# Kernel tuning notes

Hardware: AMD Instinct MI355X
Metric: run time of the kernel (lower is better)

The kernel has to match this reference:

```python
import jax, jax.numpy as jnp
import numpy as np

K_CONST = 0.005
D_U = 0.001
D_V = 0.005
LAYERS = [3, 256, 256, 256, 256, 2]
N_PTS = 131072


def setup_inputs() -> dict:
    key = jax.random.key(0)
    ks = jax.random.split(key, 3 + 2 * (len(LAYERS) - 1))
    inp = {
        "t": jax.random.uniform(ks[0], (N_PTS, 1), dtype=jnp.float32),
        "x": jax.random.uniform(ks[1], (N_PTS, 1), dtype=jnp.float32),
        "y": jax.random.uniform(ks[2], (N_PTS, 1), dtype=jnp.float32),
    }
    # PyTorch nn.Linear default init: U(-1/sqrt(fan_in), 1/sqrt(fan_in))
    for i in range(len(LAYERS) - 1):
        fan_in = LAYERS[i]
        s = 1.0 / np.sqrt(fan_in)
        inp[f"W{i}"] = jax.random.uniform(ks[3 + 2 * i], (LAYERS[i], LAYERS[i + 1]),
                                          minval=-s, maxval=s, dtype=jnp.float32)
        inp[f"b{i}"] = jax.random.uniform(ks[4 + 2 * i], (LAYERS[i + 1],),
                                          minval=-s, maxval=s, dtype=jnp.float32)
    return inp


def _mlp(params, inp):
    # inp: (3,) -> (2,) tanh MLP (tanh on all but last layer)
    h = inp
    for W, b in params[:-1]:
        h = jnp.tanh(h @ W + b)
    W, b = params[-1]
    return h @ W + b


def reference(t, x, y, W0, b0, W1, b1, W2, b2, W3, b3, W4, b4):
    params = [(W0, b0), (W1, b1), (W2, b2), (W3, b3), (W4, b4)]
    net = lambda p: _mlp(params, p)  # (3,) -> (2,)

    pts = jnp.concatenate([t, x, y], axis=1)            # (N, 3)
    uv = jax.vmap(net)(pts)                              # (N, 2)
    jac = jax.vmap(jax.jacrev(net))(pts)                 # (N, 2, 3)
    hess = jax.vmap(jax.jacfwd(jax.jacrev(net)))(pts)    # (N, 2, 3, 3)

    u = uv[:, 0:1]
    v = uv[:, 1:2]
    u_t = jac[:, 0, 0:1]
    v_t = jac[:, 1, 0:1]
    u_xx = hess[:, 0, 1, 1][:, None]
    u_yy = hess[:, 0, 2, 2][:, None]
    v_xx = hess[:, 1, 1, 1][:, None]
    v_yy = hess[:, 1, 2, 2][:, None]

    f = u - u ** 3 - K_CONST - v + D_U * (u_xx + u_yy) - u_t
    g = u - v + D_V * (v_xx + v_yy) - v_t
    return (u, v, f, g)
```

## Files before the change

kernel.cpp:

```cpp
#include <hip/hip_runtime.h>
#include <math.h>

#define N_PTS   131072
#define K_CONST 0.005f
#define D_U     0.001f
#define D_V     0.005f

typedef unsigned short u16;
typedef __attribute__((ext_vector_type(8))) _Float16 f16x8;
typedef __attribute__((ext_vector_type(4))) float    f32x4;
typedef __attribute__((ext_vector_type(4))) u16      u16x4;
typedef __attribute__((ext_vector_type(8))) u16      u16x8;

__device__ __forceinline__ u16 f2h(float x){
    _Float16 h = (_Float16)x;
    return __builtin_bit_cast(u16, h);
}
__device__ __forceinline__ float h2f(u16 h){
    return (float)__builtin_bit_cast(_Float16, h);
}

__device__ __forceinline__ float tanh_fast(float z){
    float e = __expf(2.f * z);
    return 1.f - 2.f * __builtin_amdgcn_rcpf(e + 1.f);
}

__global__ void prep_weights(const float* __restrict__ W1, const float* __restrict__ W2,
                             const float* __restrict__ W3, u16* __restrict__ ws)
{
    int gid  = blockIdx.x * 256 + threadIdx.x;
    int lane = gid & 63;
    int nt   = (gid >> 6) & 15;
    int ks   = (gid >> 10) & 7;
    int L    = gid >> 13;
    if (L >= 3) return;
    const float* W = (L == 0) ? W1 : ((L == 1) ? W2 : W3);
    int n  = nt * 16 + (lane & 15);
    int kg = lane >> 4;
    u16 h[8];
    #pragma unroll
    for (int j = 0; j < 8; ++j) {
        int k = ks * 32 + kg * 8 + j;
        h[j] = f2h(W[k * 256 + n]);
    }
    *(u16x8*)&ws[(size_t)gid * 8] = *(u16x8*)h;
}


#define KSTEP(KS, WC, WN, PN)                                                              \
  {                                                                                        \
    _Pragma("unroll")                                                                      \
    for (int nt = 0; nt < 4; ++nt)                                                         \
      WN[nt] = *(const f16x8*)((PN) + nt * 512);                                           \
    int hoff = mbase + ((64 * (KS) + 16 * kg) ^ mxor);                                     \
    f16x8 hv = *(const f16x8*)(Hb + 0 * 8192 + hoff);                                      \
    f16x8 ht = *(const f16x8*)(Hb + 1 * 8192 + hoff);                                      \
    f16x8 hx = *(const f16x8*)(Hb + 2 * 8192 + hoff);                                      \
    f16x8 hy = *(const f16x8*)(Hb + 3 * 8192 + hoff);                                      \
    f16x8 hl = *(const f16x8*)(Hb + 4 * 8192 + hoff);                                      \
    __builtin_amdgcn_s_setprio(1);                                                         \
    _Pragma("unroll")                                                                      \
    for (int nt = 0; nt < 4; ++nt) {                                                       \
      acc[0][nt] = __builtin_amdgcn_mfma_f32_16x16x32_f16(WC[nt], hv, acc[0][nt], 0, 0, 0);\
      acc[1][nt] = __builtin_amdgcn_mfma_f32_16x16x32_f16(WC[nt], ht, acc[1][nt], 0, 0, 0);\
      acc[2][nt] = __builtin_amdgcn_mfma_f32_16x16x32_f16(WC[nt], hx, acc[2][nt], 0, 0, 0);\
      acc[3][nt] = __builtin_amdgcn_mfma_f32_16x16x32_f16(WC[nt], hy, acc[3][nt], 0, 0, 0);\
      acc[4][nt] = __builtin_amdgcn_mfma_f32_16x16x32_f16(WC[nt], hl, acc[4][nt], 0, 0, 0);\
    }                                                                                      \
    __builtin_amdgcn_s_setprio(0);                                                         \
  }

__global__ __launch_bounds__(256, 2)
void pinn_mfma5(const float* __restrict__ t_in, const float* __restrict__ x_in,
                const float* __restrict__ y_in,
                const float* __restrict__ W0, const float* __restrict__ b0,
                const float* __restrict__ b1, const float* __restrict__ b2,
                const float* __restrict__ b3,
                const float* __restrict__ W4, const float* __restrict__ b4,
                const u16* __restrict__ ws,
                float* __restrict__ out)
{
    __shared__ u16 H[5 * 16 * 256];
    char* Hb = (char*)H;

    const int tid  = threadIdx.x;
    const int lane = tid & 63;
    const int wv   = tid >> 6;

    {
        int p = tid & 15, c = tid >> 4;
        int g0 = blockIdx.x * 16 + p;
        float tv = t_in[g0], xv = x_in[g0], yv = y_in[g0];
        #pragma unroll
        for (int half = 0; half < 2; ++half) {
            int n0 = c * 16 + half * 8;
            float w0[8], w1[8], w2[8], bb[8];
            #pragma unroll
            for (int q = 0; q < 2; ++q) {
                *(float4*)&w0[q*4] = *(const float4*)&W0[0*256 + n0 + q*4];
                *(float4*)&w1[q*4] = *(const float4*)&W0[1*256 + n0 + q*4];
                *(float4*)&w2[q*4] = *(const float4*)&W0[2*256 + n0 + q*4];
                *(float4*)&bb[q*4] = *(const float4*)&b0[n0 + q*4];
            }
            u16 sv[8], st[8], sx[8], sy[8], sl[8];
            #pragma unroll
            for (int j = 0; j < 8; ++j) {
                float z = tv*w0[j] + xv*w1[j] + yv*w2[j] + bb[j];
                float a = tanh_fast(z);
                float g = 1.f - a*a;
                sv[j] = f2h(a);
                st[j] = f2h(g * w0[j]);
                sx[j] = f2h(g * w1[j]);
                sy[j] = f2h(g * w2[j]);
                sl[j] = f2h(-2.f * a * g * (w1[j]*w1[j] + w2[j]*w2[j]));
            }
            int off = p * 512 + ((c * 32 + half * 16) ^ (p << 4));
            *(u16x8*)(Hb + 0*8192 + off) = *(u16x8*)sv;
            *(u16x8*)(Hb + 1*8192 + off) = *(u16x8*)st;
            *(u16x8*)(Hb + 2*8192 + off) = *(u16x8*)sx;
            *(u16x8*)(Hb + 3*8192 + off) = *(u16x8*)sy;
            *(u16x8*)(Hb + 4*8192 + off) = *(u16x8*)sl;
        }
    }
    __syncthreads();

    const int mrow  = lane & 15;
    const int kg    = lane >> 4;
    const int mxor  = mrow << 4;
    const int mbase = mrow * 512;

    const u16* pWb = ws + wv * 2048 + lane * 8;

    f16x8 whA[4], whB[4];
    #pragma unroll
    for (int nt = 0; nt < 4; ++nt)
        whA[nt] = *(const f16x8*)(pWb + nt * 512);

    #pragma unroll 1
    for (int L = 0; L < 3; ++L) {
        const float* bL = (L == 0) ? b1 : ((L == 1) ? b2 : b3);

        f32x4 acc[5][4];
        #pragma unroll
        for (int s = 0; s < 5; ++s)
            #pragma unroll
            for (int nt = 0; nt < 4; ++nt)
                acc[s][nt] = (f32x4){0.f, 0.f, 0.f, 0.f};

        const u16* pL = pWb + L * 65536;
        const int  Ln = (L < 2) ? (L + 1) : 2;
        const u16* pN = pWb + Ln * 65536;

        KSTEP(0, whA, whB, pL + 1*8192);
        KSTEP(1, whB, whA, pL + 2*8192);
        KSTEP(2, whA, whB, pL + 3*8192);
        KSTEP(3, whB, whA, pL + 4*8192);
        KSTEP(4, whA, whB, pL + 5*8192);
        KSTEP(5, whB, whA, pL + 6*8192);
        KSTEP(6, whA, whB, pL + 7*8192);
        KSTEP(7, whB, whA, pN);

        __syncthreads();

        #pragma unroll
        for (int nt = 0; nt < 4; ++nt) {
            int nb = (wv * 4 + nt) * 16 + kg * 4;
            float4 bv = *(const float4*)&bL[nb];
            float bva[4] = {bv.x, bv.y, bv.z, bv.w};
            u16 ov[4], ot4[4], ox4[4], oy4[4], ol4[4];
            #pragma unroll
            for (int r = 0; r < 4; ++r) {
                float z0 = acc[0][nt][r] + bva[r];
                float a  = tanh_fast(z0);
                float g  = 1.f - a * a;
                float zt = acc[1][nt][r];
                float zx = acc[2][nt][r];
                float zy = acc[3][nt][r];
                float zl = acc[4][nt][r];
                ov[r]  = f2h(a);
                ot4[r] = f2h(g * zt);
                ox4[r] = f2h(g * zx);
                oy4[r] = f2h(g * zy);
                ol4[r] = f2h(g * zl - 2.f * a * g * (zx*zx + zy*zy));
            }
            int off = mbase + ((2 * nb) ^ mxor);
            *(u16x4*)(Hb + 0*8192 + off) = *(u16x4*)ov;
            *(u16x4*)(Hb + 1*8192 + off) = *(u16x4*)ot4;
            *(u16x4*)(Hb + 2*8192 + off) = *(u16x4*)ox4;
            *(u16x4*)(Hb + 3*8192 + off) = *(u16x4*)oy4;
            *(u16x4*)(Hb + 4*8192 + off) = *(u16x4*)ol4;
        }
        __syncthreads();
    }

    {
        int p = tid >> 4, i = tid & 15;
        float pu = 0.f, pv = 0.f, put = 0.f, pvt = 0.f, plu = 0.f, plv = 0.f;
        #pragma unroll
        for (int half = 0; half < 2; ++half) {
            int k0  = i * 16 + half * 8;
            int off = p * 512 + ((i * 32 + half * 16) ^ (p << 4));
            u16x8 hv = *(const u16x8*)(Hb + 0*8192 + off);
            u16x8 ht = *(const u16x8*)(Hb + 1*8192 + off);
            u16x8 hl = *(const u16x8*)(Hb + 4*8192 + off);
            float w4[16];
            #pragma unroll
            for (int q = 0; q < 4; ++q)
                *(float4*)&w4[q*4] = *(const float4*)&W4[k0 * 2 + q * 4];
            #pragma unroll
            for (int j = 0; j < 8; ++j) {
                float vv = h2f(hv[j]);
                float tt = h2f(ht[j]);
                float ll = h2f(hl[j]);
                float wa = w4[2*j], wb2 = w4[2*j + 1];
                pu  += vv * wa;  pv  += vv * wb2;
                put += tt * wa;  pvt += tt * wb2;
                plu += ll * wa;  plv += ll * wb2;
            }
        }
        #pragma unroll
        for (int m = 1; m < 16; m <<= 1) {
            pu  += __shfl_xor(pu, m);   pv  += __shfl_xor(pv, m);
            put += __shfl_xor(put, m);  pvt += __shfl_xor(pvt, m);
            plu += __shfl_xor(plu, m);  plv += __shfl_xor(plv, m);
        }
        if (i == 0) {
            float u = pu + b4[0];
            float v = pv + b4[1];
            int gpt = blockIdx.x * 16 + p;
            float fo = u - u*u*u - K_CONST - v + D_U * plu - put;
            float go = u - v + D_V * plv - pvt;
            out[0 * N_PTS + gpt] = u;
            out[1 * N_PTS + gpt] = v;
            out[2 * N_PTS + gpt] = fo;
            out[3 * N_PTS + gpt] = go;
        }
    }
}

#define PTS   16
#define NTHR  256
#define HDIM  256
#define KC    32
#define HPAD  260

__global__ __launch_bounds__(NTHR, 1)
void pinn_diffreact_f32(const float* __restrict__ t_in, const float* __restrict__ x_in,
                        const float* __restrict__ y_in,
                        const float* __restrict__ W0, const float* __restrict__ b0,
                        const float* __restrict__ W1, const float* __restrict__ b1,
                        const float* __restrict__ W2, const float* __restrict__ b2,
                        const float* __restrict__ W3, const float* __restrict__ b3,
                        const float* __restrict__ W4, const float* __restrict__ b4,
                        float* __restrict__ out)
{
    __shared__ float Hs[6 * PTS * HPAD];
    __shared__ float Wc[KC * HDIM];
    const int tid = threadIdx.x;
    const int pt = tid >> 4;
    const int fbase = (tid & 15) * 4;
    const int gpt = blockIdx.x * PTS + pt;
    {
        const float tv = t_in[gpt], xv = x_in[gpt], yv = y_in[gpt];
        #pragma unroll
        for (int jv = 0; jv < 4; ++jv)
            #pragma unroll
            for (int q = 0; q < 4; ++q) {
                const int f = fbase + jv * 64 + q;
                const float w0 = W0[f], w1 = W0[256 + f], w2 = W0[512 + f];
                const float z = tv*w0 + xv*w1 + yv*w2 + b0[f];
                const float a = tanhf(z), g = 1.f - a*a;
                Hs[(0*PTS+pt)*HPAD+f] = a;
                Hs[(1*PTS+pt)*HPAD+f] = g*w0;
                Hs[(2*PTS+pt)*HPAD+f] = g*w1;
                Hs[(3*PTS+pt)*HPAD+f] = g*w2;
                Hs[(4*PTS+pt)*HPAD+f] = -2.f*a*g*w1*w1;
                Hs[(5*PTS+pt)*HPAD+f] = -2.f*a*g*w2*w2;
            }
    }
    __syncthreads();
    const float* Ws[3] = {W1, W2, W3};
    const float* bs[3] = {b1, b2, b3};
    for (int L = 0; L < 3; ++L) {
        const float* __restrict__ W = Ws[L];
        const float* __restrict__ b = bs[L];
        float acc[6][16];
        #pragma unroll
        for (int s = 0; s < 6; ++s)
            #pragma unroll
            for (int j = 0; j < 16; ++j) acc[s][j] = 0.f;
        for (int kc = 0; kc < HDIM / KC; ++kc) {
            __syncthreads();
            const float4* src = (const float4*)(W + kc * KC * HDIM);
            float4* dst = (float4*)Wc;
            #pragma unroll
            for (int i2 = 0; i2 < (KC * HDIM / 4) / NTHR; ++i2)
                dst[tid + i2 * NTHR] = src[tid + i2 * NTHR];
            __syncthreads();
            #pragma unroll
            for (int k4 = 0; k4 < KC; k4 += 4) {
                float4 h[6];
                #pragma unroll
                for (int s = 0; s < 6; ++s)
                    h[s] = *(const float4*)&Hs[(s*PTS+pt)*HPAD + kc*KC + k4];
                #pragma unroll
                for (int q = 0; q < 4; ++q) {
                    float hv[6];
                    #pragma unroll
                    for (int s = 0; s < 6; ++s)
                        hv[s] = (q==0) ? h[s].x : (q==1) ? h[s].y : (q==2) ? h[s].z : h[s].w;
                    #pragma unroll
                    for (int jv = 0; jv < 4; ++jv) {
                        const float4 wq = *(const float4*)&Wc[(k4+q)*HDIM + fbase + jv*64];
                        const float wvv[4] = {wq.x, wq.y, wq.z, wq.w};
                        #pragma unroll
                        for (int r = 0; r < 4; ++r)
                            #pragma unroll
                            for (int s = 0; s < 6; ++s)
                                acc[s][jv*4+r] += hv[s] * wvv[r];
                    }
                }
            }
        }
        __syncthreads();
        #pragma unroll
        for (int jv = 0; jv < 4; ++jv)
            #pragma unroll
            for (int q = 0; q < 4; ++q) {
                const int j = jv*4+q, f = fbase + jv*64 + q;
                const float z = acc[0][j] + b[f];
                const float a = tanhf(z), g = 1.f - a*a;
                const float zt = acc[1][j], zx = acc[2][j], zy = acc[3][j];
                const float zxx = acc[4][j], zyy = acc[5][j];
                Hs[(0*PTS+pt)*HPAD+f] = a;
                Hs[(1*PTS+pt)*HPAD+f] = g*zt;
                Hs[(2*PTS+pt)*HPAD+f] = g*zx;
                Hs[(3*PTS+pt)*HPAD+f] = g*zy;
                Hs[(4*PTS+pt)*HPAD+f] = g*zxx - 2.f*a*g*zx*zx;
                Hs[(5*PTS+pt)*HPAD+f] = g*zyy - 2.f*a*g*zy*zy;
            }
        __syncthreads();
    }
    float p[6][2];
    #pragma unroll
    for (int s = 0; s < 6; ++s) { p[s][0] = 0.f; p[s][1] = 0.f; }
    #pragma unroll
    for (int jv = 0; jv < 4; ++jv)
        #pragma unroll
        for (int q = 0; q < 4; ++q) {
            const int f = fbase + jv*64 + q;
            const float w0 = W4[f*2], w1 = W4[f*2+1];
            #pragma unroll
            for (int s = 0; s < 6; ++s) {
                const float hv = Hs[(s*PTS+pt)*HPAD+f];
                p[s][0] += hv*w0; p[s][1] += hv*w1;
            }
        }
    #pragma unroll
    for (int m = 1; m < 16; m <<= 1)
        #pragma unroll
        for (int s = 0; s < 6; ++s) {
            p[s][0] += __shfl_xor(p[s][0], m);
            p[s][1] += __shfl_xor(p[s][1], m);
        }
    if ((tid & 15) == 0) {
        const float u = p[0][0] + b4[0];
        const float v = p[0][1] + b4[1];
        const float ut = p[1][0], vt = p[1][1];
        const float uxx = p[4][0], vxx = p[4][1];
        const float uyy = p[5][0], vyy = p[5][1];
        const float fo = u - u*u*u - K_CONST - v + D_U*(uxx+uyy) - ut;
        const float go = u - v + D_V*(vxx+vyy) - vt;
        out[0*N_PTS+gpt] = u;
        out[1*N_PTS+gpt] = v;
        out[2*N_PTS+gpt] = fo;
        out[3*N_PTS+gpt] = go;
    }
}

extern "C" void kernel_launch(void* const* d_in, const int* in_sizes, int n_in,
                              void* d_out, int out_size, void* d_ws, size_t ws_size,
                              hipStream_t stream)
{
    const float* t_in = (const float*)d_in[0];
    const float* x_in = (const float*)d_in[1];
    const float* y_in = (const float*)d_in[2];
    const float* W0 = (const float*)d_in[3];
    const float* b0 = (const float*)d_in[4];
    const float* W1 = (const float*)d_in[5];
    const float* b1 = (const float*)d_in[6];
    const float* W2 = (const float*)d_in[7];
    const float* b2 = (const float*)d_in[8];
    const float* W3 = (const float*)d_in[9];
    const float* b3 = (const float*)d_in[10];
    const float* W4 = (const float*)d_in[11];
    const float* b4 = (const float*)d_in[12];
    float* out = (float*)d_out;

    const size_t WS_NEEDED = (size_t)3 * 8 * 16 * 64 * 8 * 2;
    if (ws_size >= WS_NEEDED) {
        u16* ws = (u16*)d_ws;
        hipLaunchKernelGGL(prep_weights, dim3(96), dim3(256), 0, stream, W1, W2, W3, ws);
        hipLaunchKernelGGL(pinn_mfma5, dim3(N_PTS / 16), dim3(256), 0, stream,
                           t_in, x_in, y_in, W0, b0, b1, b2, b3, W4, b4, ws, out);
    } else {
        hipLaunchKernelGGL(pinn_diffreact_f32, dim3(N_PTS / PTS), dim3(NTHR), 0, stream,
                           t_in, x_in, y_in, W0, b0, W1, b1, W2, b2, W3, b3, W4, b4, out);
    }
}
```

Measured before the change: 289.9 us.

## Split each block's work across eight waves with two N-tiles each

Doubles the block from 256 to 512 threads, so each wave owns two 16-column output tiles instead of four. This halves per-wave accumulators and weight registers and aims for more resident waves to hide latency. The packed weight layout is reordered so each wave's tiles are contiguous, and the layer-0 and output stages are respread across 512 threads. fp16 conversion now uses packed round-toward-zero (cvt_pkrtz), which changes rounding slightly. Each 16-point block still rereads the full weight set, and more waves now share the same LDS activations.

```diff
diff --git a/kernel.cpp b/kernel.cpp
--- a/kernel.cpp
+++ b/kernel.cpp
@@ -7,10 +7,13 @@
 #define D_V     0.005f
 
 typedef unsigned short u16;
+typedef unsigned int   u32;
 typedef __attribute__((ext_vector_type(8))) _Float16 f16x8;
 typedef __attribute__((ext_vector_type(4))) float    f32x4;
 typedef __attribute__((ext_vector_type(4))) u16      u16x4;
 typedef __attribute__((ext_vector_type(8))) u16      u16x8;
+typedef __attribute__((ext_vector_type(2))) u32      u32x2;
+typedef __attribute__((ext_vector_type(4))) u32      u32x4;
 
 __device__ __forceinline__ u16 f2h(float x){
     _Float16 h = (_Float16)x;
@@ -18,6 +21,23 @@
 }
 __device__ __forceinline__ float h2f(u16 h){
     return (float)__builtin_bit_cast(_Float16, h);
+}
+__device__ __forceinline__ u32 pkrtz(float a, float b){
+    return __builtin_bit_cast(u32, __builtin_amdgcn_cvt_pkrtz(a, b));
+}
+__device__ __forceinline__ u32x2 pk4(float a, float b, float c, float d){
+    u32x2 r;
+    r.x = pkrtz(a, b);
+    r.y = pkrtz(c, d);
+    return r;
+}
+__device__ __forceinline__ u32x4 pk8(const float* v){
+    u32x4 r;
+    r.x = pkrtz(v[0], v[1]);
+    r.y = pkrtz(v[2], v[3]);
+    r.z = pkrtz(v[4], v[5]);
+    r.w = pkrtz(v[6], v[7]);
+    return r;
 }
 
 __device__ __forceinline__ float tanh_fast(float z){
@@ -43,15 +63,15 @@
         int k = ks * 32 + kg * 8 + j;
         h[j] = f2h(W[k * 256 + n]);
     }
-    *(u16x8*)&ws[(size_t)gid * 8] = *(u16x8*)h;
-}
-
-
-#define KSTEP(KS, WC, WN, PN)                                                              \
+    size_t ostore = ((size_t)((L * 16 + nt) * 8 + ks) * 64 + lane) * 8;
+    *(u16x8*)&ws[ostore] = *(u16x8*)h;
+}
+
+
+#define KSTEP(KS, WC, WN, P0, P1)                                                          \
   {                                                                                        \
-    _Pragma("unroll")                                                                      \
-    for (int nt = 0; nt < 4; ++nt)                                                         \
-      WN[nt] = *(const f16x8*)((PN) + nt * 512);                                           \
+    WN[0] = *(const f16x8*)(P0);                                                           \
+    WN[1] = *(const f16x8*)(P1);                                                           \
     int hoff = mbase + ((64 * (KS) + 16 * kg) ^ mxor);                                     \
     f16x8 hv = *(const f16x8*)(Hb + 0 * 8192 + hoff);                                      \
     f16x8 ht = *(const f16x8*)(Hb + 1 * 8192 + hoff);                                      \
@@ -60,7 +80,7 @@
     f16x8 hl = *(const f16x8*)(Hb + 4 * 8192 + hoff);                                      \
     __builtin_amdgcn_s_setprio(1);                                                         \
     _Pragma("unroll")                                                                      \
-    for (int nt = 0; nt < 4; ++nt) {                                                       \
+    for (int nt = 0; nt < 2; ++nt) {                                                       \
       acc[0][nt] = __builtin_amdgcn_mfma_f32_16x16x32_f16(WC[nt], hv, acc[0][nt], 0, 0, 0);\
       acc[1][nt] = __builtin_amdgcn_mfma_f32_16x16x32_f16(WC[nt], ht, acc[1][nt], 0, 0, 0);\
       acc[2][nt] = __builtin_amdgcn_mfma_f32_16x16x32_f16(WC[nt], hx, acc[2][nt], 0, 0, 0);\
@@ -70,8 +90,8 @@
     __builtin_amdgcn_s_setprio(0);                                                         \
   }
 
-__global__ __launch_bounds__(256, 2)
-void pinn_mfma5(const float* __restrict__ t_in, const float* __restrict__ x_in,
+__global__ __launch_bounds__(512, 4)
+void pinn_mfma6(const float* __restrict__ t_in, const float* __restrict__ x_in,
                 const float* __restrict__ y_in,
                 const float* __restrict__ W0, const float* __restrict__ b0,
                 const float* __restrict__ b1, const float* __restrict__ b2,
@@ -91,36 +111,33 @@
         int p = tid & 15, c = tid >> 4;
         int g0 = blockIdx.x * 16 + p;
         float tv = t_in[g0], xv = x_in[g0], yv = y_in[g0];
-        #pragma unroll
-        for (int half = 0; half < 2; ++half) {
-            int n0 = c * 16 + half * 8;
-            float w0[8], w1[8], w2[8], bb[8];
-            #pragma unroll
-            for (int q = 0; q < 2; ++q) {
-                *(float4*)&w0[q*4] = *(const float4*)&W0[0*256 + n0 + q*4];
-                *(float4*)&w1[q*4] = *(const float4*)&W0[1*256 + n0 + q*4];
-                *(float4*)&w2[q*4] = *(const float4*)&W0[2*256 + n0 + q*4];
-                *(float4*)&bb[q*4] = *(const float4*)&b0[n0 + q*4];
-            }
-            u16 sv[8], st[8], sx[8], sy[8], sl[8];
-            #pragma unroll
-            for (int j = 0; j < 8; ++j) {
-                float z = tv*w0[j] + xv*w1[j] + yv*w2[j] + bb[j];
-                float a = tanh_fast(z);
-                float g = 1.f - a*a;
-                sv[j] = f2h(a);
-                st[j] = f2h(g * w0[j]);
-                sx[j] = f2h(g * w1[j]);
-                sy[j] = f2h(g * w2[j]);
-                sl[j] = f2h(-2.f * a * g * (w1[j]*w1[j] + w2[j]*w2[j]));
-            }
-            int off = p * 512 + ((c * 32 + half * 16) ^ (p << 4));
-            *(u16x8*)(Hb + 0*8192 + off) = *(u16x8*)sv;
-            *(u16x8*)(Hb + 1*8192 + off) = *(u16x8*)st;
-            *(u16x8*)(Hb + 2*8192 + off) = *(u16x8*)sx;
-            *(u16x8*)(Hb + 3*8192 + off) = *(u16x8*)sy;
-            *(u16x8*)(Hb + 4*8192 + off) = *(u16x8*)sl;
-        }
+        int n0 = c * 8;
+        float w0[8], w1[8], w2[8], bb[8];
+        #pragma unroll
+        for (int q = 0; q < 2; ++q) {
+            *(float4*)&w0[q*4] = *(const float4*)&W0[0*256 + n0 + q*4];
+            *(float4*)&w1[q*4] = *(const float4*)&W0[1*256 + n0 + q*4];
+            *(float4*)&w2[q*4] = *(const float4*)&W0[2*256 + n0 + q*4];
+            *(float4*)&bb[q*4] = *(const float4*)&b0[n0 + q*4];
+        }
+        float sv[8], st[8], sx[8], sy[8], sl[8];
+        #pragma unroll
+        for (int j = 0; j < 8; ++j) {
+            float z = tv*w0[j] + xv*w1[j] + yv*w2[j] + bb[j];
+            float a = tanh_fast(z);
+            float g = 1.f - a*a;
+            sv[j] = a;
+            st[j] = g * w0[j];
+            sx[j] = g * w1[j];
+            sy[j] = g * w2[j];
+            sl[j] = -2.f * a * g * (w1[j]*w1[j] + w2[j]*w2[j]);
+        }
+        int off = p * 512 + ((2 * n0) ^ (p << 4));
+        *(u32x4*)(Hb + 0*8192 + off) = pk8(sv);
+        *(u32x4*)(Hb + 1*8192 + off) = pk8(st);
+        *(u32x4*)(Hb + 2*8192 + off) = pk8(sx);
+        *(u32x4*)(Hb + 3*8192 + off) = pk8(sy);
+        *(u32x4*)(Hb + 4*8192 + off) = pk8(sl);
     }
     __syncthreads();
 
@@ -129,45 +146,47 @@
     const int mxor  = mrow << 4;
     const int mbase = mrow * 512;
 
-    const u16* pWb = ws + wv * 2048 + lane * 8;
-
-    f16x8 whA[4], whB[4];
-    #pragma unroll
-    for (int nt = 0; nt < 4; ++nt)
-        whA[nt] = *(const f16x8*)(pWb + nt * 512);
+    const u16* pW0 = ws + (size_t)(wv * 2) * 4096 + lane * 8;
+    const u16* pW1 = pW0 + 4096;
+
+    f16x8 whA[2], whB[2];
+    whA[0] = *(const f16x8*)(pW0);
+    whA[1] = *(const f16x8*)(pW1);
 
     #pragma unroll 1
     for (int L = 0; L < 3; ++L) {
         const float* bL = (L == 0) ? b1 : ((L == 1) ? b2 : b3);
 
-        f32x4 acc[5][4];
-        #pragma unroll
-        for (int s = 0; s < 5; ++s)
-            #pragma unroll
-            for (int nt = 0; nt < 4; ++nt)
-                acc[s][nt] = (f32x4){0.f, 0.f, 0.f, 0.f};
-
-        const u16* pL = pWb + L * 65536;
-        const int  Ln = (L < 2) ? (L + 1) : 2;
-        const u16* pN = pWb + Ln * 65536;
-
-        KSTEP(0, whA, whB, pL + 1*8192);
-        KSTEP(1, whB, whA, pL + 2*8192);
-        KSTEP(2, whA, whB, pL + 3*8192);
-        KSTEP(3, whB, whA, pL + 4*8192);
-        KSTEP(4, whA, whB, pL + 5*8192);
-        KSTEP(5, whB, whA, pL + 6*8192);
-        KSTEP(6, whA, whB, pL + 7*8192);
-        KSTEP(7, whB, whA, pN);
+        f32x4 acc[5][2];
+        #pragma unroll
+        for (int s = 0; s < 5; ++s) {
+            acc[s][0] = (f32x4){0.f, 0.f, 0.f, 0.f};
+            acc[s][1] = (f32x4){0.f, 0.f, 0.f, 0.f};
+        }
+
+        const u16* pL0 = pW0 + L * 65536;
+        const u16* pL1 = pW1 + L * 65536;
+        const int  Ln  = (L < 2) ? (L + 1) : 2;
+        const u16* pN0 = pW0 + Ln * 65536;
+        const u16* pN1 = pW1 + Ln * 65536;
+
+        KSTEP(0, whA, whB, pL0 + 1*512, pL1 + 1*512);
+        KSTEP(1, whB, whA, pL0 + 2*512, pL1 + 2*512);
+        KSTEP(2, whA, whB, pL0 + 3*512, pL1 + 3*512);
+        KSTEP(3, whB, whA, pL0 + 4*512, pL1 + 4*512);
+        KSTEP(4, whA, whB, pL0 + 5*512, pL1 + 5*512);
+        KSTEP(5, whB, whA, pL0 + 6*512, pL1 + 6*512);
+        KSTEP(6, whA, whB, pL0 + 7*512, pL1 + 7*512);
+        KSTEP(7, whB, whA, pN0, pN1);
 
         __syncthreads();
 
         #pragma unroll
-        for (int nt = 0; nt < 4; ++nt) {
-            int nb = (wv * 4 + nt) * 16 + kg * 4;
+        for (int nt = 0; nt < 2; ++nt) {
+            int nb = (wv * 2 + nt) * 16 + kg * 4;
             float4 bv = *(const float4*)&bL[nb];
             float bva[4] = {bv.x, bv.y, bv.z, bv.w};
-            u16 ov[4], ot4[4], ox4[4], oy4[4], ol4[4];
+            float oa[4], ot[4], ox[4], oy[4], ol[4];
             #pragma unroll
             for (int r = 0; r < 4; ++r) {
                 float z0 = acc[0][nt][r] + bva[r];
@@ -177,49 +196,46 @@
                 float zx = acc[2][nt][r];
                 float zy = acc[3][nt][r];
                 float zl = acc[4][nt][r];
-                ov[r]  = f2h(a);
-                ot4[r] = f2h(g * zt);
-                ox4[r] = f2h(g * zx);
-                oy4[r] = f2h(g * zy);
-                ol4[r] = f2h(g * zl - 2.f * a * g * (zx*zx + zy*zy));
+                oa[r] = a;
+                ot[r] = g * zt;
+                ox[r] = g * zx;
+                oy[r] = g * zy;
+                ol[r] = g * zl - 2.f * a * g * (zx*zx + zy*zy);
             }
             int off = mbase + ((2 * nb) ^ mxor);
-            *(u16x4*)(Hb + 0*8192 + off) = *(u16x4*)ov;
-            *(u16x4*)(Hb + 1*8192 + off) = *(u16x4*)ot4;
-            *(u16x4*)(Hb + 2*8192 + off) = *(u16x4*)ox4;
-            *(u16x4*)(Hb + 3*8192 + off) = *(u16x4*)oy4;
-            *(u16x4*)(Hb + 4*8192 + off) = *(u16x4*)ol4;
+            *(u32x2*)(Hb + 0*8192 + off) = pk4(oa[0], oa[1], oa[2], oa[3]);
+            *(u32x2*)(Hb + 1*8192 + off) = pk4(ot[0], ot[1], ot[2], ot[3]);
+            *(u32x2*)(Hb + 2*8192 + off) = pk4(ox[0], ox[1], ox[2], ox[3]);
+            *(u32x2*)(Hb + 3*8192 + off) = pk4(oy[0], oy[1], oy[2], oy[3]);
+            *(u32x2*)(Hb + 4*8192 + off) = pk4(ol[0], ol[1], ol[2], ol[3]);
         }
         __syncthreads();
     }
 
     {
-        int p = tid >> 4, i = tid & 15;
+        int p = tid >> 5, i = tid & 31;
+        int k0 = i * 8;
+        int off = p * 512 + ((2 * k0) ^ (p << 4));
+        u16x8 hv = *(const u16x8*)(Hb + 0*8192 + off);
+        u16x8 ht = *(const u16x8*)(Hb + 1*8192 + off);
+        u16x8 hl = *(const u16x8*)(Hb + 4*8192 + off);
+        float w4[16];
+        #pragma unroll
+        for (int q = 0; q < 4; ++q)
+            *(float4*)&w4[q*4] = *(const float4*)&W4[k0 * 2 + q * 4];
         float pu = 0.f, pv = 0.f, put = 0.f, pvt = 0.f, plu = 0.f, plv = 0.f;
         #pragma unroll
-        for (int half = 0; half < 2; ++half) {
-            int k0  = i * 16 + half * 8;
-            int off = p * 512 + ((i * 32 + half * 16) ^ (p << 4));
-            u16x8 hv = *(const u16x8*)(Hb + 0*8192 + off);
-            u16x8 ht = *(const u16x8*)(Hb + 1*8192 + off);
-            u16x8 hl = *(const u16x8*)(Hb + 4*8192 + off);
-            float w4[16];
-            #pragma unroll
-            for (int q = 0; q < 4; ++q)
-                *(float4*)&w4[q*4] = *(const float4*)&W4[k0 * 2 + q * 4];
-            #pragma unroll
-            for (int j = 0; j < 8; ++j) {
-                float vv = h2f(hv[j]);
-                float tt = h2f(ht[j]);
-                float ll = h2f(hl[j]);
-                float wa = w4[2*j], wb2 = w4[2*j + 1];
-                pu  += vv * wa;  pv  += vv * wb2;
-                put += tt * wa;  pvt += tt * wb2;
-                plu += ll * wa;  plv += ll * wb2;
-            }
-        }
-        #pragma unroll
-        for (int m = 1; m < 16; m <<= 1) {
+        for (int j = 0; j < 8; ++j) {
+            float vv = h2f(hv[j]);
+            float tt = h2f(ht[j]);
+            float ll = h2f(hl[j]);
+            float wa = w4[2*j], wb2 = w4[2*j + 1];
+            pu  += vv * wa;  pv  += vv * wb2;
+            put += tt * wa;  pvt += tt * wb2;
+            plu += ll * wa;  plv += ll * wb2;
+        }
+        #pragma unroll
+        for (int m = 1; m < 32; m <<= 1) {
             pu  += __shfl_xor(pu, m);   pv  += __shfl_xor(pv, m);
             put += __shfl_xor(put, m);  pvt += __shfl_xor(pvt, m);
             plu += __shfl_xor(plu, m);  plv += __shfl_xor(plv, m);
@@ -401,7 +417,7 @@
     if (ws_size >= WS_NEEDED) {
         u16* ws = (u16*)d_ws;
         hipLaunchKernelGGL(prep_weights, dim3(96), dim3(256), 0, stream, W1, W2, W3, ws);
-        hipLaunchKernelGGL(pinn_mfma5, dim3(N_PTS / 16), dim3(256), 0, stream,
+        hipLaunchKernelGGL(pinn_mfma6, dim3(N_PTS / 16), dim3(512), 0, stream,
                            t_in, x_in, y_in, W0, b0, b1, b2, b3, W4, b4, ws, out);
     } else {
         hipLaunchKernelGGL(pinn_diffreact_f32, dim3(N_PTS / PTS), dim3(NTHR), 0, stream,
```

Result: no change. 291.6 us (+0.6%).
